# Performance work log

Hardware: AMD Instinct MI355X
Metric: run time of the kernel (lower is better)

## Reference

```python
import jax, jax.numpy as jnp
import numpy as np

SCALE = 1.0 / np.sqrt(64.0).astype(np.float32)  # module hardcodes 64**0.5

def setup_inputs() -> dict:
    key = jax.random.key(0)
    kx, kw = jax.random.split(key)
    B, S, D, O = 8, 2048, 768, 768
    x = jax.random.normal(kx, (B, S, D), dtype=jnp.float32)
    # keras 'uniform' initializer: U(-0.05, 0.05)
    kernel = jax.random.uniform(kw, (3, D, O), dtype=jnp.float32, minval=-0.05, maxval=0.05)
    return {"x": x, "kernel": kernel}

def reference(x, kernel):
    # x: [B,S,D], kernel: [3,D,O]
    WQ = jnp.einsum('bsd,do->bso', x, kernel[0])
    WK = jnp.einsum('bsd,do->bso', x, kernel[1])
    WV = jnp.einsum('bsd,do->bso', x, kernel[2])
    QK = jnp.einsum('bso,bto->bst', WQ, WK) * SCALE  # [B,S,S]
    A = jax.nn.softmax(QK, axis=-1)
    return jnp.einsum('bst,bto->bso', A, WV)
```

## Files before the change

### kernel.cpp

```cpp
#include <hip/hip_runtime.h>


typedef _Float16 f16;
typedef _Float16 f16x8 __attribute__((ext_vector_type(8)));
typedef _Float16 f16x4 __attribute__((ext_vector_type(4)));
typedef float f32x4 __attribute__((ext_vector_type(4)));

__device__ __forceinline__ void gload16(const void* g, void* l) {
    __builtin_amdgcn_global_load_lds((__attribute__((address_space(1))) void*)g,
                                     (__attribute__((address_space(3))) void*)l,
                                     16, 0, 0);
}

template <int MODE, typename OutT>
__global__ __launch_bounds__(256, 2)
void gemm_bt(const f16* __restrict__ A, const f16* __restrict__ B,
             OutT* __restrict__ C, float* R, int K, int lda, int ldb, int ldc,
             long sA, long sB, long sC)
{
    __shared__ __align__(16) f16 lA[128 * 64];
    __shared__ __align__(16) f16 lB[128 * 64];

    const int tid  = threadIdx.x;
    const int wave = tid >> 6;
    const int lane = tid & 63;

    const unsigned gx = gridDim.x, gy = gridDim.y;
    const unsigned nb = gx * gy * gridDim.z;
    unsigned lin = blockIdx.x + gx * (blockIdx.y + gy * blockIdx.z);
    if ((nb & 7u) == 0u) lin = (lin & 7u) * (nb >> 3) + (lin >> 3);
    const unsigned bx = lin % gx;
    const unsigned rem = lin / gx;
    const unsigned by = rem % gy;
    const unsigned bz = rem / gy;

    A += (long)bz * sA;
    B += (long)bz * sB;
    C += (long)bz * sC;

    const long row0 = (long)by * 128;
    const long col0 = (long)bx * 128;

    const int r0 = tid >> 3;
    const int cs = (((tid & 7) ^ (r0 & 7)) * 8);
    const f16* ag0 = A + (row0 +      r0) * lda + cs;
    const f16* ag1 = A + (row0 + 32 + r0) * lda + cs;
    const f16* ag2 = A + (row0 + 64 + r0) * lda + cs;
    const f16* ag3 = A + (row0 + 96 + r0) * lda + cs;
    const f16* bg0 = B + (col0 +      r0) * ldb + cs;
    const f16* bg1 = B + (col0 + 32 + r0) * ldb + cs;
    const f16* bg2 = B + (col0 + 64 + r0) * ldb + cs;
    const f16* bg3 = B + (col0 + 96 + r0) * ldb + cs;
    f16* lA0 = lA +        wave * 512;
    f16* lA1 = lA + 2048 + wave * 512;
    f16* lA2 = lA + 4096 + wave * 512;
    f16* lA3 = lA + 6144 + wave * 512;
    f16* lB0 = lB +        wave * 512;
    f16* lB1 = lB + 2048 + wave * 512;
    f16* lB2 = lB + 4096 + wave * 512;
    f16* lB3 = lB + 6144 + wave * 512;

    const int wm = wave >> 1, wn = wave & 1;
    const int fl = lane & 15;
    const int q  = lane >> 4;
    const int co = ((q ^ (fl & 7)) * 8);
    const f16* paw = lA + (wm * 64 + fl) * 64;
    const f16* pbw = lB + (wn * 64 + fl) * 64;

    f32x4 acc[4][4] = {};

    for (int k0 = 0; k0 < K; k0 += 64) {
        __syncthreads();
        gload16(ag0, lA0); gload16(ag1, lA1);
        gload16(ag2, lA2); gload16(ag3, lA3);
        gload16(bg0, lB0); gload16(bg1, lB1);
        gload16(bg2, lB2); gload16(bg3, lB3);
        ag0 += 64; ag1 += 64; ag2 += 64; ag3 += 64;
        bg0 += 64; bg1 += 64; bg2 += 64; bg3 += 64;
        __syncthreads();

#pragma unroll
        for (int kk = 0; kk < 64; kk += 32) {
            const int o = co ^ (kk == 0 ? 0 : 32);
            f16x8 a[4], b[4];
#pragma unroll
            for (int i = 0; i < 4; ++i)
                a[i] = *(const f16x8*)(paw + i * 1024 + o);
#pragma unroll
            for (int j = 0; j < 4; ++j)
                b[j] = *(const f16x8*)(pbw + j * 1024 + o);
#pragma unroll
            for (int i = 0; i < 4; ++i)
#pragma unroll
                for (int j = 0; j < 4; ++j)
                    acc[i][j] = __builtin_amdgcn_mfma_f32_16x16x32_f16(
                        a[i], b[j], acc[i][j], 0, 0, 0);
        }
    }

    const int rq = (lane >> 4) * 4;
    if (MODE != 0) R += (long)bz * 2048;
#pragma unroll
    for (int i = 0; i < 4; ++i) {
#pragma unroll
        for (int r = 0; r < 4; ++r) {
            const long row = row0 + wm * 64 + i * 16 + rq + r;
            if (MODE == 0) {
#pragma unroll
                for (int j = 0; j < 4; ++j) {
                    const long col = col0 + wn * 64 + j * 16 + fl;
                    C[row * ldc + col] = (OutT)acc[i][j][r];
                }
            } else if (MODE == 1) {
                float s = 0.f;
#pragma unroll
                for (int j = 0; j < 4; ++j) {
                    const long col = col0 + wn * 64 + j * 16 + fl;
                    float e = __expf(acc[i][j][r] * 0.125f - 12.0f);
                    C[row * ldc + col] = (OutT)e;
                    s += e;
                }
                s += __shfl_xor(s, 1, 16);
                s += __shfl_xor(s, 2, 16);
                s += __shfl_xor(s, 4, 16);
                s += __shfl_xor(s, 8, 16);
                if (fl == 0) atomicAdd(&R[row], s);
            } else {
                const float inv = 1.0f / R[row];
#pragma unroll
                for (int j = 0; j < 4; ++j) {
                    const long col = col0 + wn * 64 + j * 16 + fl;
                    C[row * ldc + col] = (OutT)(acc[i][j][r] * inv);
                }
            }
        }
    }
}

__global__ void cvt_f32_f16(const float* __restrict__ in, f16* __restrict__ out,
                            int n4)
{
    int i = blockIdx.x * blockDim.x + threadIdx.x;
    int stride = gridDim.x * blockDim.x;
    for (; i < n4; i += stride) {
        float4 v = ((const float4*)in)[i];
        f16x4 h;
        h[0] = (f16)v.x; h[1] = (f16)v.y; h[2] = (f16)v.z; h[3] = (f16)v.w;
        ((f16x4*)out)[i] = h;
    }
}

__global__ void wtrans(const float* __restrict__ w, f16* __restrict__ wT)
{
    __shared__ float t[32][33];
    const int h  = blockIdx.z;
    const int o0 = blockIdx.x * 32, d0 = blockIdx.y * 32;
    const int tx = threadIdx.x & 31, ty = threadIdx.x >> 5;
    const float* src = w + ((size_t)h * 768 + d0) * 768 + o0;
#pragma unroll
    for (int r = 0; r < 32; r += 8)
        t[ty + r][tx] = src[(size_t)(ty + r) * 768 + tx];
    __syncthreads();
    f16* dst = wT + ((size_t)h * 768 + o0) * 768 + d0;
#pragma unroll
    for (int r = 0; r < 32; r += 8)
        dst[(size_t)(ty + r) * 768 + tx] = (f16)t[tx][ty + r];
}

extern "C" void kernel_launch(void* const* d_in, const int* in_sizes, int n_in,
                              void* d_out, int out_size, void* d_ws, size_t ws_size,
                              hipStream_t stream)
{
    (void)in_sizes; (void)n_in; (void)out_size; (void)ws_size;
    const float* x = (const float*)d_in[0];
    const float* w = (const float*)d_in[1];
    float* out = (float*)d_out;

    const long NX = 12582912;
    const long NW = 1769472;
    f16* xh  = (f16*)d_ws;
    f16* wT  = xh + NX;
    f16* QKh = wT + NW;
    f16* Vt  = QKh + 2 * NX;
    f16* Sc  = Vt + NX;
    float* R = (float*)xh;

    cvt_f32_f16<<<2048, 256, 0, stream>>>(x, xh, (int)(NX / 4));
    wtrans<<<dim3(24, 24, 3), 256, 0, stream>>>(w, wT);

    gemm_bt<0, f16><<<dim3(12, 128, 1), 256, 0, stream>>>(
        xh, wT, QKh, nullptr, 768, 768, 768, 1536, 0, 0, 0);
    gemm_bt<0, f16><<<dim3(16, 6, 8), 256, 0, stream>>>(
        wT + 1179648, xh, Vt, nullptr, 768, 768, 768, 2048, 0, 1572864, 1572864);
    hipMemsetAsync(R, 0, 8 * 2048 * sizeof(float), stream);
    gemm_bt<1, f16><<<dim3(16, 16, 8), 256, 0, stream>>>(
        QKh, QKh + 768, Sc, R, 768, 1536, 1536, 2048, 3145728, 3145728, 4194304);
    gemm_bt<2, float><<<dim3(6, 16, 8), 256, 0, stream>>>(
        Sc, Vt, out, R, 2048, 2048, 2048, 768, 4194304, 1572864, 1572864);
}
```

Baseline: 304.0 us.

## Triple-buffer LDS loads with 256x128 tiles and 512-thread GEMM blocks

The GEMM kernel now uses 512-thread blocks computing 256x128 output tiles, with three LDS buffers filled by async global_load_lds. Prefetch runs two k-steps ahead, gated by vmcnt waits and one barrier per iteration instead of two. MFMA sections are wrapped in s_setprio so matrix math gets issue priority. The aim is to hide global-to-LDS latency and reuse more data per block, at the cost of about 144KB of LDS, which likely limits occupancy to one block per CU.

```diff
diff --git a/kernel.cpp b/kernel.cpp
--- a/kernel.cpp
+++ b/kernel.cpp
@@ -13,13 +13,13 @@
 }
 
 template <int MODE, typename OutT>
-__global__ __launch_bounds__(256, 2)
+__global__ __launch_bounds__(512, 2)
 void gemm_bt(const f16* __restrict__ A, const f16* __restrict__ B,
              OutT* __restrict__ C, float* R, int K, int lda, int ldb, int ldc,
              long sA, long sB, long sC)
 {
-    __shared__ __align__(16) f16 lA[128 * 64];
-    __shared__ __align__(16) f16 lB[128 * 64];
+    __shared__ __align__(16) f16 lA[3 * 16384];
+    __shared__ __align__(16) f16 lB[3 * 8192];
 
     const int tid  = threadIdx.x;
     const int wave = tid >> 6;
@@ -38,65 +38,72 @@
     B += (long)bz * sB;
     C += (long)bz * sC;
 
-    const long row0 = (long)by * 128;
+    const long row0 = (long)by * 256;
     const long col0 = (long)bx * 128;
 
     const int r0 = tid >> 3;
     const int cs = (((tid & 7) ^ (r0 & 7)) * 8);
-    const f16* ag0 = A + (row0 +      r0) * lda + cs;
-    const f16* ag1 = A + (row0 + 32 + r0) * lda + cs;
-    const f16* ag2 = A + (row0 + 64 + r0) * lda + cs;
-    const f16* ag3 = A + (row0 + 96 + r0) * lda + cs;
-    const f16* bg0 = B + (col0 +      r0) * ldb + cs;
-    const f16* bg1 = B + (col0 + 32 + r0) * ldb + cs;
-    const f16* bg2 = B + (col0 + 64 + r0) * ldb + cs;
-    const f16* bg3 = B + (col0 + 96 + r0) * ldb + cs;
-    f16* lA0 = lA +        wave * 512;
-    f16* lA1 = lA + 2048 + wave * 512;
-    f16* lA2 = lA + 4096 + wave * 512;
-    f16* lA3 = lA + 6144 + wave * 512;
-    f16* lB0 = lB +        wave * 512;
-    f16* lB1 = lB + 2048 + wave * 512;
-    f16* lB2 = lB + 4096 + wave * 512;
-    f16* lB3 = lB + 6144 + wave * 512;
+    const f16* ag0 = A + (row0 +       r0) * lda + cs;
+    const f16* ag1 = A + (row0 +  64 + r0) * lda + cs;
+    const f16* ag2 = A + (row0 + 128 + r0) * lda + cs;
+    const f16* ag3 = A + (row0 + 192 + r0) * lda + cs;
+    const f16* bg0 = B + (col0 +       r0) * ldb + cs;
+    const f16* bg1 = B + (col0 +  64 + r0) * ldb + cs;
+
+#define STAGE(dA, dB) do {                                                    \
+        gload16(ag0, (dA) +         tid * 8);                                 \
+        gload16(ag1, (dA) +  4096 + tid * 8);                                 \
+        gload16(ag2, (dA) +  8192 + tid * 8);                                 \
+        gload16(ag3, (dA) + 12288 + tid * 8);                                 \
+        gload16(bg0, (dB) +         tid * 8);                                 \
+        gload16(bg1, (dB) +  4096 + tid * 8);                                 \
+        ag0 += 64; ag1 += 64; ag2 += 64; ag3 += 64; bg0 += 64; bg1 += 64;     \
+    } while (0)
 
     const int wm = wave >> 1, wn = wave & 1;
     const int fl = lane & 15;
     const int q  = lane >> 4;
     const int co = ((q ^ (fl & 7)) * 8);
-    const f16* paw = lA + (wm * 64 + fl) * 64;
-    const f16* pbw = lB + (wn * 64 + fl) * 64;
 
     f32x4 acc[4][4] = {};
-
-    for (int k0 = 0; k0 < K; k0 += 64) {
-        __syncthreads();
-        gload16(ag0, lA0); gload16(ag1, lA1);
-        gload16(ag2, lA2); gload16(ag3, lA3);
-        gload16(bg0, lB0); gload16(bg1, lB1);
-        gload16(bg2, lB2); gload16(bg3, lB3);
-        ag0 += 64; ag1 += 64; ag2 += 64; ag3 += 64;
-        bg0 += 64; bg1 += 64; bg2 += 64; bg3 += 64;
-        __syncthreads();
-
-#pragma unroll
-        for (int kk = 0; kk < 64; kk += 32) {
-            const int o = co ^ (kk == 0 ? 0 : 32);
+    const int nt = K >> 6;
+
+    STAGE(lA, lB);
+    if (nt > 1) STAGE(lA + 16384, lB + 8192);
+
+    int cb = 0;
+    for (int t = 0; t < nt; ++t) {
+        if (t + 1 < nt) { asm volatile("s_waitcnt vmcnt(6)" ::: "memory"); }
+        else            { asm volatile("s_waitcnt vmcnt(0)" ::: "memory"); }
+        __builtin_amdgcn_s_barrier();
+
+        const int nb2 = cb ? cb - 1 : 2;
+        if (t + 2 < nt) STAGE(lA + nb2 * 16384, lB + nb2 * 8192);
+
+        const f16* pa = lA + cb * 16384 + (wm * 64 + fl) * 64;
+        const f16* pb = lB + cb * 8192  + (wn * 64 + fl) * 64;
+#pragma unroll
+        for (int kk = 0; kk < 2; ++kk) {
+            const int o = co ^ (kk << 5);
             f16x8 a[4], b[4];
 #pragma unroll
             for (int i = 0; i < 4; ++i)
-                a[i] = *(const f16x8*)(paw + i * 1024 + o);
+                a[i] = *(const f16x8*)(pa + i * 1024 + o);
 #pragma unroll
             for (int j = 0; j < 4; ++j)
-                b[j] = *(const f16x8*)(pbw + j * 1024 + o);
+                b[j] = *(const f16x8*)(pb + j * 1024 + o);
+            __builtin_amdgcn_s_setprio(1);
 #pragma unroll
             for (int i = 0; i < 4; ++i)
 #pragma unroll
                 for (int j = 0; j < 4; ++j)
                     acc[i][j] = __builtin_amdgcn_mfma_f32_16x16x32_f16(
                         a[i], b[j], acc[i][j], 0, 0, 0);
+            __builtin_amdgcn_s_setprio(0);
         }
+        cb = cb == 2 ? 0 : cb + 1;
     }
+#undef STAGE
 
     const int rq = (lane >> 4) * 4;
     if (MODE != 0) R += (long)bz * 2048;
@@ -188,13 +195,13 @@
     cvt_f32_f16<<<2048, 256, 0, stream>>>(x, xh, (int)(NX / 4));
     wtrans<<<dim3(24, 24, 3), 256, 0, stream>>>(w, wT);
 
-    gemm_bt<0, f16><<<dim3(12, 128, 1), 256, 0, stream>>>(
+    gemm_bt<0, f16><<<dim3(12, 64, 1), 512, 0, stream>>>(
         xh, wT, QKh, nullptr, 768, 768, 768, 1536, 0, 0, 0);
-    gemm_bt<0, f16><<<dim3(16, 6, 8), 256, 0, stream>>>(
+    gemm_bt<0, f16><<<dim3(16, 3, 8), 512, 0, stream>>>(
         wT + 1179648, xh, Vt, nullptr, 768, 768, 768, 2048, 0, 1572864, 1572864);
     hipMemsetAsync(R, 0, 8 * 2048 * sizeof(float), stream);
-    gemm_bt<1, f16><<<dim3(16, 16, 8), 256, 0, stream>>>(
+    gemm_bt<1, f16><<<dim3(16, 8, 8), 512, 0, stream>>>(
         QKh, QKh + 768, Sc, R, 768, 1536, 1536, 2048, 3145728, 3145728, 4194304);
-    gemm_bt<2, float><<<dim3(6, 16, 8), 256, 0, stream>>>(
+    gemm_bt<2, float><<<dim3(6, 8, 8), 512, 0, stream>>>(
         Sc, Vt, out, R, 2048, 2048, 2048, 768, 4194304, 1572864, 1572864);
 }
```

Measured after the change: 386.8 us. 27.2% more time.

## Fold Q and K projections into a single precomputed Wq·Wkᵀ matrix

Applied to the files above, without the earlier changes.

Uses the identity QKᵀ = X (Wq Wkᵀ) Xᵀ. A small 768x768 product G = Wq·Wkᵀ (scaled by 1/8) is computed first, and then only one projection X·G is formed instead of the two projections Q and K. The scores GEMM then multiplies XG directly against the fp16 input X. This removes one full B·S·D·D projection GEMM and halves the intermediate write, at the cost of a tiny extra GEMM and an extra fp16 rounding of G, which can affect accuracy.

```diff
diff --git a/kernel.cpp b/kernel.cpp
--- a/kernel.cpp
+++ b/kernel.cpp
@@ -16,7 +16,7 @@
 __global__ __launch_bounds__(256, 2)
 void gemm_bt(const f16* __restrict__ A, const f16* __restrict__ B,
              OutT* __restrict__ C, float* R, int K, int lda, int ldb, int ldc,
-             long sA, long sB, long sC)
+             long sA, long sB, long sC, float oscale)
 {
     __shared__ __align__(16) f16 lA[128 * 64];
     __shared__ __align__(16) f16 lB[128 * 64];
@@ -109,14 +109,14 @@
 #pragma unroll
                 for (int j = 0; j < 4; ++j) {
                     const long col = col0 + wn * 64 + j * 16 + fl;
-                    C[row * ldc + col] = (OutT)acc[i][j][r];
+                    C[row * ldc + col] = (OutT)(acc[i][j][r] * oscale);
                 }
             } else if (MODE == 1) {
                 float s = 0.f;
 #pragma unroll
                 for (int j = 0; j < 4; ++j) {
                     const long col = col0 + wn * 64 + j * 16 + fl;
-                    float e = __expf(acc[i][j][r] * 0.125f - 12.0f);
+                    float e = __expf(acc[i][j][r] - 12.0f);
                     C[row * ldc + col] = (OutT)e;
                     s += e;
                 }
@@ -153,15 +153,14 @@
 __global__ void wtrans(const float* __restrict__ w, f16* __restrict__ wT)
 {
     __shared__ float t[32][33];
-    const int h  = blockIdx.z;
     const int o0 = blockIdx.x * 32, d0 = blockIdx.y * 32;
     const int tx = threadIdx.x & 31, ty = threadIdx.x >> 5;
-    const float* src = w + ((size_t)h * 768 + d0) * 768 + o0;
+    const float* src = w + (size_t)d0 * 768 + o0;
 #pragma unroll
     for (int r = 0; r < 32; r += 8)
         t[ty + r][tx] = src[(size_t)(ty + r) * 768 + tx];
     __syncthreads();
-    f16* dst = wT + ((size_t)h * 768 + o0) * 768 + d0;
+    f16* dst = wT + (size_t)o0 * 768 + d0;
 #pragma unroll
     for (int r = 0; r < 32; r += 8)
         dst[(size_t)(ty + r) * 768 + tx] = (f16)t[tx][ty + r];
@@ -178,23 +177,29 @@
 
     const long NX = 12582912;
     const long NW = 1769472;
+    const long NW1 = 589824;
     f16* xh  = (f16*)d_ws;
-    f16* wT  = xh + NX;
-    f16* QKh = wT + NW;
-    f16* Vt  = QKh + 2 * NX;
+    f16* wh  = xh + NX;
+    f16* wt2 = wh + NW;
+    f16* GT  = wt2 + NW1;
+    f16* XG  = GT + NW1;
+    f16* Vt  = XG + NX;
     f16* Sc  = Vt + NX;
-    float* R = (float*)xh;
+    float* R = (float*)wh;
 
     cvt_f32_f16<<<2048, 256, 0, stream>>>(x, xh, (int)(NX / 4));
-    wtrans<<<dim3(24, 24, 3), 256, 0, stream>>>(w, wT);
-
-    gemm_bt<0, f16><<<dim3(12, 128, 1), 256, 0, stream>>>(
-        xh, wT, QKh, nullptr, 768, 768, 768, 1536, 0, 0, 0);
+    cvt_f32_f16<<<1024, 256, 0, stream>>>(w, wh, (int)(NW / 4));
+    wtrans<<<dim3(24, 24, 1), 256, 0, stream>>>(w + 2 * NW1, wt2);
+
+    gemm_bt<0, f16><<<dim3(6, 6, 1), 256, 0, stream>>>(
+        wh + NW1, wh, GT, nullptr, 768, 768, 768, 768, 0, 0, 0, 0.125f);
+    gemm_bt<0, f16><<<dim3(6, 128, 1), 256, 0, stream>>>(
+        xh, GT, XG, nullptr, 768, 768, 768, 768, 0, 0, 0, 1.0f);
     gemm_bt<0, f16><<<dim3(16, 6, 8), 256, 0, stream>>>(
-        wT + 1179648, xh, Vt, nullptr, 768, 768, 768, 2048, 0, 1572864, 1572864);
+        wt2, xh, Vt, nullptr, 768, 768, 768, 2048, 0, 1572864, 1572864, 1.0f);
     hipMemsetAsync(R, 0, 8 * 2048 * sizeof(float), stream);
     gemm_bt<1, f16><<<dim3(16, 16, 8), 256, 0, stream>>>(
-        QKh, QKh + 768, Sc, R, 768, 1536, 1536, 2048, 3145728, 3145728, 4194304);
+        XG, xh, Sc, R, 768, 768, 768, 2048, 1572864, 1572864, 4194304, 1.0f);
     gemm_bt<2, float><<<dim3(6, 16, 8), 256, 0, stream>>>(
-        Sc, Vt, out, R, 2048, 2048, 2048, 768, 4194304, 1572864, 1572864);
-}
+        Sc, Vt, out, R, 2048, 2048, 2048, 768, 4194304, 1572864, 1572864, 1.0f);
+}
```

After: 297.0 us. 1.02x faster.
